# Kernel tuning notes

Hardware: AMD Instinct MI355X
Metric: run time of the kernel (lower is better)

Reference implementation:

```python
import jax, jax.numpy as jnp
import numpy as np

B = 4096      # number of query nodes (len(samp_neighs))
U = 50000     # number of unique sampled neighbor nodes
D = 300       # node feature dim (GloVe-style ConceptNet embeddings)
E = 131072    # total (node, neighbor) pairs, avg degree ~32


def setup_inputs() -> dict:
    key = jax.random.key(0)
    k1, k2, k3 = jax.random.split(key, 3)
    row_idx = jnp.sort(jax.random.randint(k1, (E,), 0, B, dtype=jnp.int64 if jax.config.jax_enable_x64 else jnp.int32)).astype(jnp.int32)
    col_idx = jax.random.randint(k2, (E,), 0, U).astype(jnp.int32)
    embed_matrix = jax.random.normal(k3, (U, D), dtype=jnp.float32)
    return {"row_idx": row_idx, "col_idx": col_idx, "embed_matrix": embed_matrix}


def reference(row_idx, col_idx, embed_matrix):
    # Build dense neighbor-membership mask [B, U]; .set (not .add) mirrors the
    # original's set semantics (duplicate neighbors count once).
    mask = jnp.zeros((B, U), dtype=embed_matrix.dtype).at[row_idx, col_idx].set(1.0)
    num_neigh = mask.sum(axis=1, keepdims=True)            # [B, 1]
    mask = mask / jnp.clip(num_neigh, 1e-8)                # row-normalize (mean)
    to_feats = mask @ embed_matrix                         # [B, D] mean aggregation
    return to_feats
```

## Files before the change

kernel.cpp:

```cpp
#include <hip/hip_runtime.h>


#define DFEAT  300
#define NCHUNK 75
#define COLS_CAP 512
#define NWAVE  4

__global__ __launch_bounds__(256) void build_rowptr(
    const int* __restrict__ row_idx, int E, int B, int* __restrict__ row_ptr)
{
    const int e = blockIdx.x * 256 + threadIdx.x;
    if (e >= E) return;
    const int r     = row_idx[e];
    const int rprev = (e == 0) ? -1 : row_idx[e - 1];
    for (int x = rprev + 1; x <= r; ++x) row_ptr[x] = e;
    if (e == E - 1) {
        for (int x = r + 1; x <= B; ++x) row_ptr[x] = E;
    }
}

__global__ __launch_bounds__(256) void mean_agg_kernel(
    const int* __restrict__ row_ptr,
    const int* __restrict__ col_idx,
    const float* __restrict__ embed,
    float* __restrict__ out)
{
    const int b    = blockIdx.x;
    const int tid  = threadIdx.x;
    const int t    = tid & 63;
    const int wave = tid >> 6;

    const int start = row_ptr[b];
    const int deg   = row_ptr[b + 1] - start;

    __shared__ int   s_cols[COLS_CAP];
    __shared__ int   s_uniq[COLS_CAP];
    __shared__ int   s_cnt;
    __shared__ float s_part[NWAVE][DFEAT];

    if (tid == 0) s_cnt = 0;
    for (int k = tid; k < deg && k < COLS_CAP; k += 256) s_cols[k] = col_idx[start + k];
    __syncthreads();

    for (int k = tid; k < deg; k += 256) {
        const int c = (k < COLS_CAP) ? s_cols[k] : col_idx[start + k];
        bool dup = false;
        for (int i = 0; i < k; ++i) {
            const int ci = (i < COLS_CAP) ? s_cols[i] : col_idx[start + i];
            dup |= (ci == c);
        }
        if (!dup) {
            const int p = atomicAdd(&s_cnt, 1);
            if (p < COLS_CAP) s_uniq[p] = c;
        }
    }
    __syncthreads();
    const int cnt = s_cnt;

    float4 acc0 = {0.f, 0.f, 0.f, 0.f};
    float4 acc1 = {0.f, 0.f, 0.f, 0.f};
    const bool hi_lane = (t < NCHUNK - 64);

    int u = wave;
    for (; u + NWAVE < cnt; u += 2 * NWAVE) {
        const float4* __restrict__ p0 = (const float4*)(embed + (long long)s_uniq[u] * DFEAT);
        const float4* __restrict__ p1 = (const float4*)(embed + (long long)s_uniq[u + NWAVE] * DFEAT);
        const float4 x0 = p0[t];
        const float4 y0 = p1[t];
        acc0.x += x0.x; acc0.y += x0.y; acc0.z += x0.z; acc0.w += x0.w;
        acc0.x += y0.x; acc0.y += y0.y; acc0.z += y0.z; acc0.w += y0.w;
        if (hi_lane) {
            const float4 x1 = p0[t + 64];
            const float4 y1 = p1[t + 64];
            acc1.x += x1.x; acc1.y += x1.y; acc1.z += x1.z; acc1.w += x1.w;
            acc1.x += y1.x; acc1.y += y1.y; acc1.z += y1.z; acc1.w += y1.w;
        }
    }
    if (u < cnt) {
        const float4* __restrict__ p0 = (const float4*)(embed + (long long)s_uniq[u] * DFEAT);
        const float4 x0 = p0[t];
        acc0.x += x0.x; acc0.y += x0.y; acc0.z += x0.z; acc0.w += x0.w;
        if (hi_lane) {
            const float4 x1 = p0[t + 64];
            acc1.x += x1.x; acc1.y += x1.y; acc1.z += x1.z; acc1.w += x1.w;
        }
    }

    *(float4*)&s_part[wave][4 * t] = acc0;
    if (hi_lane) *(float4*)&s_part[wave][256 + 4 * t] = acc1;
    __syncthreads();

    if (tid < NCHUNK) {
        const float scale = (cnt > 0) ? (1.0f / (float)cnt) : 0.0f;
        const int o = 4 * tid;
        float4 r = {0.f, 0.f, 0.f, 0.f};
        #pragma unroll
        for (int w = 0; w < NWAVE; ++w) {
            const float4 p = *(const float4*)&s_part[w][o];
            r.x += p.x; r.y += p.y; r.z += p.z; r.w += p.w;
        }
        r.x *= scale; r.y *= scale; r.z *= scale; r.w *= scale;
        *(float4*)(out + (long long)b * DFEAT + o) = r;
    }
}

extern "C" void kernel_launch(void* const* d_in, const int* in_sizes, int n_in,
                              void* d_out, int out_size, void* d_ws, size_t ws_size,
                              hipStream_t stream) {
    const int*   row_idx = (const int*)  d_in[0];
    const int*   col_idx = (const int*)  d_in[1];
    const float* embed   = (const float*)d_in[2];
    float*       out     = (float*)      d_out;

    const int E = in_sizes[0];
    const int B = out_size / DFEAT;

    int* row_ptr = (int*)d_ws;

    build_rowptr<<<(E + 255) / 256, 256, 0, stream>>>(row_idx, E, B, row_ptr);
    mean_agg_kernel<<<B, 256, 0, stream>>>(row_ptr, col_idx, embed, out);
}
```

Before: 112.2 us.

## Assign one wavefront per row with ballot-based dedup and no block syncs

```diff
diff --git a/kernel.cpp b/kernel.cpp
--- a/kernel.cpp
+++ b/kernel.cpp
@@ -3,8 +3,8 @@
 
 #define DFEAT  300
 #define NCHUNK 75
-#define COLS_CAP 512
-#define NWAVE  4
+#define CAP    128
+#define WPB    4
 
 __global__ __launch_bounds__(256) void build_rowptr(
     const int* __restrict__ row_idx, int E, int B, int* __restrict__ row_ptr)
@@ -23,84 +23,89 @@
     const int* __restrict__ row_ptr,
     const int* __restrict__ col_idx,
     const float* __restrict__ embed,
-    float* __restrict__ out)
+    float* __restrict__ out,
+    int B)
 {
-    const int b    = blockIdx.x;
-    const int tid  = threadIdx.x;
-    const int t    = tid & 63;
-    const int wave = tid >> 6;
+    const int lane = threadIdx.x & 63;
+    const int w    = threadIdx.x >> 6;
+    const int b    = blockIdx.x * WPB + w;
+    if (b >= B) return;
+
+    __shared__ int s_uniq[WPB][CAP];
 
     const int start = row_ptr[b];
     const int deg   = row_ptr[b + 1] - start;
 
-    __shared__ int   s_cols[COLS_CAP];
-    __shared__ int   s_uniq[COLS_CAP];
-    __shared__ int   s_cnt;
-    __shared__ float s_part[NWAVE][DFEAT];
+    int cnt = 0;
+    for (int base = 0; base < deg; base += 64) {
+        const int  i     = base + lane;
+        const bool valid = (i < deg);
+        const int  c     = valid ? col_idx[start + i] : -1;
 
-    if (tid == 0) s_cnt = 0;
-    for (int k = tid; k < deg && k < COLS_CAP; k += 256) s_cols[k] = col_idx[start + k];
-    __syncthreads();
+        bool dup = false;
+        for (int q = 0; q < cnt; ++q) dup = dup || (s_uniq[w][q] == c);
+        const int jmax = (deg - base - 1 < 63) ? (deg - base - 1) : 63;
+        for (int j = 0; j < jmax; ++j) {
+            const int cj = __shfl(c, j);
+            dup = dup || ((j < lane) && (cj == c));
+        }
 
-    for (int k = tid; k < deg; k += 256) {
-        const int c = (k < COLS_CAP) ? s_cols[k] : col_idx[start + k];
-        bool dup = false;
-        for (int i = 0; i < k; ++i) {
-            const int ci = (i < COLS_CAP) ? s_cols[i] : col_idx[start + i];
-            dup |= (ci == c);
+        const unsigned long long m = __ballot(valid && !dup);
+        const int rank = __popcll(m & ((1ull << lane) - 1ull));
+        if (valid && !dup) {
+            const int p = cnt + rank;
+            if (p < CAP) s_uniq[w][p] = c;
         }
-        if (!dup) {
-            const int p = atomicAdd(&s_cnt, 1);
-            if (p < COLS_CAP) s_uniq[p] = c;
+        cnt += (int)__popcll(m);
+    }
+    if (cnt > CAP) cnt = CAP;
+
+    const bool hi = (lane < NCHUNK - 64);
+    float4 a0 = {0.f, 0.f, 0.f, 0.f};
+    float4 a1 = {0.f, 0.f, 0.f, 0.f};
+
+    int u = 0;
+    for (; u + 4 <= cnt; u += 4) {
+        const float4* __restrict__ p0 = (const float4*)(embed + (size_t)s_uniq[w][u    ] * DFEAT);
+        const float4* __restrict__ p1 = (const float4*)(embed + (size_t)s_uniq[w][u + 1] * DFEAT);
+        const float4* __restrict__ p2 = (const float4*)(embed + (size_t)s_uniq[w][u + 2] * DFEAT);
+        const float4* __restrict__ p3 = (const float4*)(embed + (size_t)s_uniq[w][u + 3] * DFEAT);
+        const float4 v0 = p0[lane];
+        const float4 v1 = p1[lane];
+        const float4 v2 = p2[lane];
+        const float4 v3 = p3[lane];
+        if (hi) {
+            const float4 h0 = p0[lane + 64];
+            const float4 h1 = p1[lane + 64];
+            const float4 h2 = p2[lane + 64];
+            const float4 h3 = p3[lane + 64];
+            a1.x += h0.x + h1.x + h2.x + h3.x;
+            a1.y += h0.y + h1.y + h2.y + h3.y;
+            a1.z += h0.z + h1.z + h2.z + h3.z;
+            a1.w += h0.w + h1.w + h2.w + h3.w;
         }
+        a0.x += v0.x + v1.x + v2.x + v3.x;
+        a0.y += v0.y + v1.y + v2.y + v3.y;
+        a0.z += v0.z + v1.z + v2.z + v3.z;
+        a0.w += v0.w + v1.w + v2.w + v3.w;
     }
-    __syncthreads();
-    const int cnt = s_cnt;
-
-    float4 acc0 = {0.f, 0.f, 0.f, 0.f};
-    float4 acc1 = {0.f, 0.f, 0.f, 0.f};
-    const bool hi_lane = (t < NCHUNK - 64);
-
-    int u = wave;
-    for (; u + NWAVE < cnt; u += 2 * NWAVE) {
-        const float4* __restrict__ p0 = (const float4*)(embed + (long long)s_uniq[u] * DFEAT);
-        const float4* __restrict__ p1 = (const float4*)(embed + (long long)s_uniq[u + NWAVE] * DFEAT);
-        const float4 x0 = p0[t];
-        const float4 y0 = p1[t];
-        acc0.x += x0.x; acc0.y += x0.y; acc0.z += x0.z; acc0.w += x0.w;
-        acc0.x += y0.x; acc0.y += y0.y; acc0.z += y0.z; acc0.w += y0.w;
-        if (hi_lane) {
-            const float4 x1 = p0[t + 64];
-            const float4 y1 = p1[t + 64];
-            acc1.x += x1.x; acc1.y += x1.y; acc1.z += x1.z; acc1.w += x1.w;
-            acc1.x += y1.x; acc1.y += y1.y; acc1.z += y1.z; acc1.w += y1.w;
-        }
-    }
-    if (u < cnt) {
-        const float4* __restrict__ p0 = (const float4*)(embed + (long long)s_uniq[u] * DFEAT);
-        const float4 x0 = p0[t];
-        acc0.x += x0.x; acc0.y += x0.y; acc0.z += x0.z; acc0.w += x0.w;
-        if (hi_lane) {
-            const float4 x1 = p0[t + 64];
-            acc1.x += x1.x; acc1.y += x1.y; acc1.z += x1.z; acc1.w += x1.w;
+    for (; u < cnt; ++u) {
+        const float4* __restrict__ p0 = (const float4*)(embed + (size_t)s_uniq[w][u] * DFEAT);
+        const float4 v0 = p0[lane];
+        a0.x += v0.x; a0.y += v0.y; a0.z += v0.z; a0.w += v0.w;
+        if (hi) {
+            const float4 h0 = p0[lane + 64];
+            a1.x += h0.x; a1.y += h0.y; a1.z += h0.z; a1.w += h0.w;
         }
     }
 
-    *(float4*)&s_part[wave][4 * t] = acc0;
-    if (hi_lane) *(float4*)&s_part[wave][256 + 4 * t] = acc1;
-    __syncthreads();
-
-    if (tid < NCHUNK) {
-        const float scale = (cnt > 0) ? (1.0f / (float)cnt) : 0.0f;
-        const int o = 4 * tid;
-        float4 r = {0.f, 0.f, 0.f, 0.f};
-        #pragma unroll
-        for (int w = 0; w < NWAVE; ++w) {
-            const float4 p = *(const float4*)&s_part[w][o];
-            r.x += p.x; r.y += p.y; r.z += p.z; r.w += p.w;
-        }
-        r.x *= scale; r.y *= scale; r.z *= scale; r.w *= scale;
-        *(float4*)(out + (long long)b * DFEAT + o) = r;
+    const float s = (cnt > 0) ? (1.0f / (float)cnt) : 0.0f;
+    float4* __restrict__ orow = (float4*)(out + (size_t)b * DFEAT);
+    float4 r0; r0.x = a0.x * s; r0.y = a0.y * s; r0.z = a0.z * s; r0.w = a0.w * s;
+    orow[lane] = r0;
+    if (hi) {
+        float4 r1; r1.x = a1.x * s; r1.y = a1.y * s; r1.z = a1.z * s; r1.w = a1.w * s;
+        orow[lane + 64] = r1;
     }
 }
 
@@ -118,5 +123,5 @@
     int* row_ptr = (int*)d_ws;
 
     build_rowptr<<<(E + 255) / 256, 256, 0, stream>>>(row_idx, E, B, row_ptr);
-    mean_agg_kernel<<<B, 256, 0, stream>>>(row_ptr, col_idx, embed, out);
+    mean_agg_kernel<<<(B + WPB - 1) / WPB, 256, 0, stream>>>(row_ptr, col_idx, embed, out, B);
 }
```

Result: no change. 111.5 us (-0.7%).
